# Performance work log

Measured on AMD Instinct MI355X. Metric: run time of the kernel, lower is better.

## Reference

```python
import jax, jax.numpy as jnp
import numpy as np

D_IN = 1024
D_OUT = 1024
N_HEADS = 16

def setup_inputs() -> dict:
    key = jax.random.key(0)
    ks = jax.random.split(key, 6)
    s = 0.02
    return {
        "x": jax.random.normal(ks[0], (4, 2048, D_IN), dtype=jnp.float32),
        "Wq": jax.random.normal(ks[1], (D_IN, D_OUT), dtype=jnp.float32) * s,
        "Wk": jax.random.normal(ks[2], (D_IN, D_OUT), dtype=jnp.float32) * s,
        "Wv": jax.random.normal(ks[3], (D_IN, D_OUT), dtype=jnp.float32) * s,
        "Wo": jax.random.normal(ks[4], (D_OUT, D_OUT), dtype=jnp.float32) * s,
        "bo": jax.random.normal(ks[5], (D_OUT,), dtype=jnp.float32) * s,
    }

def reference(x, Wq, Wk, Wv, Wo, bo):
    b, n, _ = x.shape
    hd = D_OUT // N_HEADS
    # project and split heads -> [b, h, n, hd]
    def split(t):
        return t.reshape(b, n, N_HEADS, hd).transpose(0, 2, 1, 3)
    q = split(x @ Wq)
    k = split(x @ Wk)
    v = split(x @ Wv)
    scores = jnp.einsum('bhqd,bhkd->bhqk', q, k)  # [b,h,n,n]
    causal = jnp.tril(jnp.ones((n, n), dtype=bool))
    scores = jnp.where(causal, scores, -jnp.inf)
    attn = jax.nn.softmax(scores / jnp.sqrt(jnp.float32(hd)), axis=-1)
    ctx = jnp.einsum('bhqk,bhkd->bhqd', attn, v)  # [b,h,n,hd]
    ctx = ctx.transpose(0, 2, 1, 3).reshape(b, n, D_OUT)
    return ctx @ Wo + bo
```

## Files before the change

kernel.cpp:

```cpp
#include <hip/hip_runtime.h>
#include <stdint.h>

typedef unsigned short u16;
typedef __attribute__((ext_vector_type(8))) short frag8;
typedef __attribute__((ext_vector_type(4))) float f32x4;
typedef __attribute__((ext_vector_type(4))) unsigned short u16x4;

#define MFMA_BF16(a,b,c) __builtin_amdgcn_mfma_f32_16x16x32_bf16((a),(b),(c),0,0,0)
#define SMSCALE 0.18033688011112042f

__device__ __forceinline__ u16 f2bf(float f) {
  union { float f; uint32_t u; } c; c.f = f;
  uint32_t u = c.u;
  uint32_t r = (u + 0x7fffu + ((u >> 16) & 1u)) >> 16;
  return (u16)r;
}

__device__ __forceinline__ uint32_t pack_bf16(float a, float b) {
  uint32_t au = __float_as_uint(a) + 0x8000u;
  uint32_t bu = __float_as_uint(b) + 0x8000u;
  return __builtin_amdgcn_perm(bu, au, 0x07060302u);
}

__device__ __forceinline__ void async16(const void* g, void* l) {
  __builtin_amdgcn_global_load_lds((const __attribute__((address_space(1))) void*)g,
                                   (__attribute__((address_space(3))) void*)l,
                                   16, 0, 0);
}

__global__ __launch_bounds__(256) void k_convert_x(const float4* __restrict__ x,
                                                   u16* __restrict__ xb) {
  int i = blockIdx.x * 256 + threadIdx.x;
  float4 v = x[i];
  u16x4 o;
  o.x = f2bf(v.x); o.y = f2bf(v.y); o.z = f2bf(v.z); o.w = f2bf(v.w);
  *(u16x4*)(xb + (size_t)i * 4) = o;
}

__global__ __launch_bounds__(256) void k_transpose_w4(
    const float* __restrict__ W0, const float* __restrict__ W1,
    const float* __restrict__ W2, const float* __restrict__ W3,
    u16* __restrict__ D0, u16* __restrict__ D1,
    u16* __restrict__ D2, u16* __restrict__ D3) {
  __shared__ float tile[64][65];
  const int z = blockIdx.z;
  const float* src = (z == 0) ? W0 : (z == 1) ? W1 : (z == 2) ? W2 : W3;
  u16* dst = (z == 0) ? D0 : (z == 1) ? D1 : (z == 2) ? D2 : D3;
  const int bx = blockIdx.x * 64;
  const int by = blockIdx.y * 64;
  const int t = threadIdx.x;
  const int tc = (t & 15) * 4;
  const int tr = t >> 4;
  #pragma unroll
  for (int p = 0; p < 4; ++p) {
    int r = tr + p * 16;
    float4 v = *(const float4*)(src + (size_t)(bx + r) * 1024 + by + tc);
    tile[r][tc + 0] = v.x; tile[r][tc + 1] = v.y;
    tile[r][tc + 2] = v.z; tile[r][tc + 3] = v.w;
  }
  __syncthreads();
  #pragma unroll
  for (int p = 0; p < 4; ++p) {
    int r = tr + p * 16;
    u16x4 o;
    o.x = f2bf(tile[tc + 0][r]);
    o.y = f2bf(tile[tc + 1][r]);
    o.z = f2bf(tile[tc + 2][r]);
    o.w = f2bf(tile[tc + 3][r]);
    *(u16x4*)(dst + (size_t)(by + r) * 1024 + bx + tc) = o;
  }
}

__global__ __launch_bounds__(256, 2) void k_gemm_qkv(const u16* __restrict__ xb,
    const u16* __restrict__ Wqt, const u16* __restrict__ Wkt, const u16* __restrict__ Wvt,
    u16* __restrict__ Qg, u16* __restrict__ Kg, u16* __restrict__ Vtg) {
  __shared__ __attribute__((aligned(16))) u16 smem[4 * 128 * 64];
  u16* T = smem;
  const int m0 = blockIdx.x * 128, n0 = blockIdx.y * 128;
  const int t = threadIdx.x, lane = t & 63, wv = t >> 6;
  const int lm = lane & 15, quad = lane >> 4;
  const int wr = wv >> 1, wc = wv & 1;
  f32x4 acc[3][4][4] = {};

  for (int k0 = 0; k0 < 1024; k0 += 64) {
    #pragma unroll
    for (int it = 0; it < 4; ++it) {
      int chunk = it * 256 + t;
      int r = chunk >> 3;
      int sc = ((chunk & 7) ^ (r & 7)) * 8;
      async16(xb + (size_t)(m0 + r) * 1024 + k0 + sc,
              smem + (size_t)(it * 256 + wv * 64) * 8);
    }
    #pragma unroll
    for (int z = 0; z < 3; ++z) {
      const u16* Bt = (z == 0) ? Wqt : (z == 1) ? Wkt : Wvt;
      #pragma unroll
      for (int it = 0; it < 4; ++it) {
        int chunk = it * 256 + t;
        int r = chunk >> 3;
        int sc = ((chunk & 7) ^ (r & 7)) * 8;
        async16(Bt + (size_t)(n0 + r) * 1024 + k0 + sc,
                smem + (size_t)((z + 1) * 1024 + it * 256 + wv * 64) * 8);
      }
    }
    __syncthreads();
    #pragma unroll
    for (int kk = 0; kk < 2; ++kk) {
      frag8 a[4];
      #pragma unroll
      for (int i = 0; i < 4; ++i) {
        int row = wr * 64 + i * 16 + lm;
        a[i] = *(const frag8*)(smem + row * 64 + (((kk * 4 + quad) ^ (row & 7)) * 8));
      }
      #pragma unroll
      for (int z = 0; z < 3; ++z) {
        #pragma unroll
        for (int j = 0; j < 4; ++j) {
          int row = wc * 64 + j * 16 + lm;
          frag8 b = *(const frag8*)(smem + (z + 1) * 8192 + row * 64 +
                                    (((kk * 4 + quad) ^ (row & 7)) * 8));
          #pragma unroll
          for (int i = 0; i < 4; ++i)
            acc[z][i][j] = MFMA_BF16(a[i], b, acc[z][i][j]);
        }
      }
    }
    __syncthreads();
  }

  #pragma unroll
  for (int z = 0; z < 2; ++z) {
    u16* tgt = z ? Kg : Qg;
    const float sc = z ? 1.0f : SMSCALE;
    #pragma unroll
    for (int i = 0; i < 4; ++i)
      #pragma unroll
      for (int j = 0; j < 4; ++j) {
        const int col = n0 + wc * 64 + j * 16 + lm;
        const int h = col >> 6, d = col & 63;
        #pragma unroll
        for (int reg = 0; reg < 4; ++reg) {
          const int row = m0 + wr * 64 + i * 16 + quad * 4 + reg;
          const int bb = row >> 11, nn = row & 2047;
          tgt[(((size_t)bb * 16 + h) * 2048 + nn) * 64 + d] = f2bf(acc[z][i][j][reg] * sc);
        }
      }
  }
  {
    const int bb = m0 >> 11, nn0 = m0 & 2047;
    const int h0 = n0 >> 6;
    #pragma unroll
    for (int p = 0; p < 2; ++p) {
      if (wc == p) {
        #pragma unroll
        for (int i = 0; i < 4; ++i)
          #pragma unroll
          for (int j = 0; j < 4; ++j) {
            const int rT = j * 16 + lm;
            #pragma unroll
            for (int reg = 0; reg < 4; ++reg) {
              const int cT = wr * 64 + i * 16 + quad * 4 + reg;
              T[rT * 136 + cT] = f2bf(acc[2][i][j][reg]);
            }
          }
      }
      __syncthreads();
      #pragma unroll
      for (int cc = 0; cc < 4; ++cc) {
        int chunk = cc * 256 + t;
        int r = chunk >> 4, tk = (chunk & 15) * 8;
        frag8 v = *(const frag8*)(T + r * 136 + tk);
        *(frag8*)(Vtg + (((size_t)bb * 16 + h0 + p) * 64 + r) * 2048 + nn0 + tk) = v;
      }
      __syncthreads();
    }
  }
}

__device__ __forceinline__ void attn_tile(const u16* Ks, const u16* Vts, u16* PsW,
                                          const frag8 aq[2], f32x4 o[4], float& l_run,
                                          int lm, int quad, int wv, bool diag) {
  f32x4 s[4];
  #pragma unroll
  for (int kt = 0; kt < 4; ++kt) {
    f32x4 z = {0.f, 0.f, 0.f, 0.f};
    #pragma unroll
    for (int dd = 0; dd < 2; ++dd) {
      frag8 ak = *(const frag8*)(Ks + (kt * 16 + lm) * 64 + (((dd * 4 + quad) ^ (lm & 7)) * 8));
      z = MFMA_BF16(ak, aq[dd], z);
    }
    s[kt] = z;
  }
  if (diag) {
    #pragma unroll
    for (int kt = 0; kt < 4; ++kt)
      #pragma unroll
      for (int rg = 0; rg < 4; ++rg)
        if (kt * 16 + quad * 4 + rg > wv * 16 + lm) s[kt][rg] = -3.0e38f;
  }
  float rs = 0.f;
  #pragma unroll
  for (int kt = 0; kt < 4; ++kt) {
    float p0 = exp2f(s[kt][0]);
    float p1 = exp2f(s[kt][1]);
    float p2 = exp2f(s[kt][2]);
    float p3 = exp2f(s[kt][3]);
    rs += (p0 + p1) + (p2 + p3);
    *(uint32_t*)(PsW + lm * 72 + kt * 16 + quad * 4)     = pack_bf16(p0, p1);
    *(uint32_t*)(PsW + lm * 72 + kt * 16 + quad * 4 + 2) = pack_bf16(p2, p3);
  }
  l_run += rs;
  #pragma unroll
  for (int ks = 0; ks < 2; ++ks) {
    frag8 bp = *(const frag8*)(PsW + lm * 72 + ks * 32 + quad * 8);
    #pragma unroll
    for (int dt = 0; dt < 4; ++dt) {
      frag8 av = *(const frag8*)(Vts + (dt * 16 + lm) * 64 + (((ks * 4 + quad) ^ (lm & 7)) * 8));
      o[dt] = MFMA_BF16(av, bp, o[dt]);
    }
  }
}

__global__ __launch_bounds__(256, 5) void k_attn(const u16* __restrict__ Qg,
                                                 const u16* __restrict__ Kg,
                                                 const u16* __restrict__ Vtg,
                                                 u16* __restrict__ ctx) {
  __shared__ __attribute__((aligned(16))) u16 Ks[64 * 64];
  __shared__ __attribute__((aligned(16))) u16 Vts[64 * 64];
  __shared__ __attribute__((aligned(16))) u16 Ps[4 * 16 * 72];
  const int bid = blockIdx.x;
  const int pair = bid >> 6;
  const int bh = ((bid >> 3) & 7) * 8 + (bid & 7);
  const int t = threadIdx.x, lane = t & 63, wv = t >> 6;
  const int lm = lane & 15, quad = lane >> 4;
  const int b = bh >> 4, h = bh & 15;
  u16* const PsW = Ps + wv * (16 * 72);

  #pragma unroll
  for (int phase = 0; phase < 2; ++phase) {
    const int qt = phase ? (31 - pair) : pair;

    frag8 aq[2];
    {
      const u16* qp = Qg + ((size_t)bh * 2048 + qt * 64 + wv * 16 + lm) * 64 + quad * 8;
      aq[0] = *(const frag8*)(qp);
      aq[1] = *(const frag8*)(qp + 32);
    }
    float l = 0.f;
    f32x4 o[4] = {};

    for (int kt0 = 0; kt0 <= qt; ++kt0) {
      #pragma unroll
      for (int it = 0; it < 2; ++it) {
        int chunk = it * 256 + t;
        int r = chunk >> 3, c = chunk & 7;
        int sc = (c ^ (r & 7)) * 8;
        async16(Kg  + ((size_t)bh * 2048 + kt0 * 64 + r) * 64 + sc, Ks  + (size_t)(it * 256 + wv * 64) * 8);
        async16(Vtg + ((size_t)bh * 64 + r) * 2048 + kt0 * 64 + sc, Vts + (size_t)(it * 256 + wv * 64) * 8);
      }
      __syncthreads();
      attn_tile(Ks, Vts, PsW, aq, o, l, lm, quad, wv, kt0 == qt);
      __syncthreads();
    }

    l += __shfl_xor(l, 16);
    l += __shfl_xor(l, 32);
    const float inv = 1.0f / l;
    #pragma unroll
    for (int dt = 0; dt < 4; ++dt) {
      *(uint32_t*)(PsW + lm * 72 + dt * 16 + quad * 4)     = pack_bf16(o[dt][0] * inv, o[dt][1] * inv);
      *(uint32_t*)(PsW + lm * 72 + dt * 16 + quad * 4 + 2) = pack_bf16(o[dt][2] * inv, o[dt][3] * inv);
    }
    const int rr = lane >> 2, cc = (lane & 3) * 8;
    const size_t row = (size_t)b * 2048 + qt * 64 + wv * 16 + rr;
    #pragma unroll
    for (int half = 0; half < 2; ++half) {
      frag8 vo = *(const frag8*)(PsW + rr * 72 + cc + half * 32);
      *(frag8*)(ctx + row * 1024 + h * 64 + cc + half * 32) = vo;
    }
  }
}

__global__ __launch_bounds__(256) void k_gemm_out(const u16* __restrict__ ctx,
    const u16* __restrict__ Wot, const float* __restrict__ bo, float* __restrict__ out) {
  __shared__ __attribute__((aligned(16))) u16 As[128 * 64];
  __shared__ __attribute__((aligned(16))) u16 Bs[128 * 64];
  const int m0 = blockIdx.x * 128, n0 = blockIdx.y * 128;
  const int t = threadIdx.x, lane = t & 63, wv = t >> 6;
  const int lm = lane & 15, quad = lane >> 4;
  const int wr = wv >> 1, wc = wv & 1;
  f32x4 acc[4][4] = {};
  for (int k0 = 0; k0 < 1024; k0 += 64) {
    #pragma unroll
    for (int it = 0; it < 4; ++it) {
      int chunk = it * 256 + t;
      int r = chunk >> 3;
      int sc = ((chunk & 7) ^ (r & 7)) * 8;
      async16(ctx + (size_t)(m0 + r) * 1024 + k0 + sc, As + (size_t)(it * 256 + wv * 64) * 8);
      async16(Wot + (size_t)(n0 + r) * 1024 + k0 + sc, Bs + (size_t)(it * 256 + wv * 64) * 8);
    }
    __syncthreads();
    #pragma unroll
    for (int kk = 0; kk < 2; ++kk) {
      frag8 a[4];
      #pragma unroll
      for (int i = 0; i < 4; ++i) {
        int row = wr * 64 + i * 16 + lm;
        a[i] = *(const frag8*)(As + row * 64 + (((kk * 4 + quad) ^ (row & 7)) * 8));
      }
      #pragma unroll
      for (int j = 0; j < 4; ++j) {
        int row = wc * 64 + j * 16 + lm;
        frag8 b = *(const frag8*)(Bs + row * 64 + (((kk * 4 + quad) ^ (row & 7)) * 8));
        #pragma unroll
        for (int i = 0; i < 4; ++i)
          acc[i][j] = MFMA_BF16(a[i], b, acc[i][j]);
      }
    }
    __syncthreads();
  }
  #pragma unroll
  for (int i = 0; i < 4; ++i)
    #pragma unroll
    for (int j = 0; j < 4; ++j) {
      const int col = n0 + wc * 64 + j * 16 + lm;
      const float bias = bo[col];
      #pragma unroll
      for (int reg = 0; reg < 4; ++reg) {
        const int row = m0 + wr * 64 + i * 16 + quad * 4 + reg;
        out[(size_t)row * 1024 + col] = acc[i][j][reg] + bias;
      }
    }
}

extern "C" void kernel_launch(void* const* d_in, const int* in_sizes, int n_in,
                              void* d_out, int out_size, void* d_ws, size_t ws_size,
                              hipStream_t stream) {
  const float* x  = (const float*)d_in[0];
  const float* Wq = (const float*)d_in[1];
  const float* Wk = (const float*)d_in[2];
  const float* Wv = (const float*)d_in[3];
  const float* Wo = (const float*)d_in[4];
  const float* bo = (const float*)d_in[5];
  float* out = (float*)d_out;
  char* ws = (char*)d_ws;

  u16* xb   = (u16*)(ws);
  u16* Wqt  = (u16*)(ws + ((size_t)16 << 20));
  u16* Wkt  = (u16*)(ws + ((size_t)18 << 20));
  u16* Wvt  = (u16*)(ws + ((size_t)20 << 20));
  u16* Wot  = (u16*)(ws + ((size_t)22 << 20));
  u16* Qg   = (u16*)(ws + ((size_t)24 << 20));
  u16* Kg   = (u16*)(ws + ((size_t)40 << 20));
  u16* Vtg  = (u16*)(ws + ((size_t)56 << 20));
  u16* ctxb = (u16*)(ws + ((size_t)72 << 20));

  k_convert_x<<<8192, 256, 0, stream>>>((const float4*)x, xb);
  k_transpose_w4<<<dim3(16, 16, 4), 256, 0, stream>>>(Wq, Wk, Wv, Wo, Wqt, Wkt, Wvt, Wot);
  k_gemm_qkv<<<dim3(64, 8), 256, 0, stream>>>(xb, Wqt, Wkt, Wvt, Qg, Kg, Vtg);
  k_attn<<<1024, 256, 0, stream>>>(Qg, Kg, Vtg, ctxb);
  k_gemm_out<<<dim3(64, 8), 256, 0, stream>>>(ctxb, Wot, bo, out);
}
```

Before: 238.1 us.

## Process four query tiles per attention block with double-buffered K/V staging

Each attention block now handles four query tiles (two from the start and two from the end of the causal range) and shares every staged K/V tile among them, so K/V loads and LDS fragment reads are reused across queries. K/V staging is double-buffered so the next tile loads while the current one is computed, leaving one barrier per iteration. The grid is halved to 512 blocks and launch bounds drop to 2 blocks per CU, trading occupancy and more registers (four sets of Q fragments and accumulators) for data reuse and overlap.

Measured after the change: 232.9 us. 2.2% less time.

```diff
diff --git a/kernel.cpp b/kernel.cpp
--- a/kernel.cpp
+++ b/kernel.cpp
@@ -177,102 +177,128 @@
   }
 }
 
-__device__ __forceinline__ void attn_tile(const u16* Ks, const u16* Vts, u16* PsW,
-                                          const frag8 aq[2], f32x4 o[4], float& l_run,
-                                          int lm, int quad, int wv, bool diag) {
-  f32x4 s[4];
-  #pragma unroll
-  for (int kt = 0; kt < 4; ++kt) {
-    f32x4 z = {0.f, 0.f, 0.f, 0.f};
-    #pragma unroll
-    for (int dd = 0; dd < 2; ++dd) {
-      frag8 ak = *(const frag8*)(Ks + (kt * 16 + lm) * 64 + (((dd * 4 + quad) ^ (lm & 7)) * 8));
-      z = MFMA_BF16(ak, aq[dd], z);
-    }
-    s[kt] = z;
-  }
-  if (diag) {
-    #pragma unroll
-    for (int kt = 0; kt < 4; ++kt)
-      #pragma unroll
-      for (int rg = 0; rg < 4; ++rg)
-        if (kt * 16 + quad * 4 + rg > wv * 16 + lm) s[kt][rg] = -3.0e38f;
-  }
-  float rs = 0.f;
-  #pragma unroll
-  for (int kt = 0; kt < 4; ++kt) {
-    float p0 = exp2f(s[kt][0]);
-    float p1 = exp2f(s[kt][1]);
-    float p2 = exp2f(s[kt][2]);
-    float p3 = exp2f(s[kt][3]);
-    rs += (p0 + p1) + (p2 + p3);
-    *(uint32_t*)(PsW + lm * 72 + kt * 16 + quad * 4)     = pack_bf16(p0, p1);
-    *(uint32_t*)(PsW + lm * 72 + kt * 16 + quad * 4 + 2) = pack_bf16(p2, p3);
-  }
-  l_run += rs;
-  #pragma unroll
-  for (int ks = 0; ks < 2; ++ks) {
-    frag8 bp = *(const frag8*)(PsW + lm * 72 + ks * 32 + quad * 8);
-    #pragma unroll
-    for (int dt = 0; dt < 4; ++dt) {
-      frag8 av = *(const frag8*)(Vts + (dt * 16 + lm) * 64 + (((ks * 4 + quad) ^ (lm & 7)) * 8));
-      o[dt] = MFMA_BF16(av, bp, o[dt]);
-    }
-  }
-}
-
-__global__ __launch_bounds__(256, 5) void k_attn(const u16* __restrict__ Qg,
+__global__ __launch_bounds__(256, 2) void k_attn(const u16* __restrict__ Qg,
                                                  const u16* __restrict__ Kg,
                                                  const u16* __restrict__ Vtg,
                                                  u16* __restrict__ ctx) {
-  __shared__ __attribute__((aligned(16))) u16 Ks[64 * 64];
-  __shared__ __attribute__((aligned(16))) u16 Vts[64 * 64];
+  __shared__ __attribute__((aligned(16))) u16 Ks[2][64 * 64];
+  __shared__ __attribute__((aligned(16))) u16 Vts[2][64 * 64];
   __shared__ __attribute__((aligned(16))) u16 Ps[4 * 16 * 72];
   const int bid = blockIdx.x;
-  const int pair = bid >> 6;
+  const int ib = bid >> 6;
   const int bh = ((bid >> 3) & 7) * 8 + (bid & 7);
+  const int qts[4] = {2 * ib, 2 * ib + 1, 30 - 2 * ib, 31 - 2 * ib};
   const int t = threadIdx.x, lane = t & 63, wv = t >> 6;
   const int lm = lane & 15, quad = lane >> 4;
   const int b = bh >> 4, h = bh & 15;
   u16* const PsW = Ps + wv * (16 * 72);
 
-  #pragma unroll
-  for (int phase = 0; phase < 2; ++phase) {
-    const int qt = phase ? (31 - pair) : pair;
-
-    frag8 aq[2];
-    {
-      const u16* qp = Qg + ((size_t)bh * 2048 + qt * 64 + wv * 16 + lm) * 64 + quad * 8;
-      aq[0] = *(const frag8*)(qp);
-      aq[1] = *(const frag8*)(qp + 32);
-    }
-    float l = 0.f;
-    f32x4 o[4] = {};
-
-    for (int kt0 = 0; kt0 <= qt; ++kt0) {
-      #pragma unroll
-      for (int it = 0; it < 2; ++it) {
-        int chunk = it * 256 + t;
-        int r = chunk >> 3, c = chunk & 7;
-        int sc = (c ^ (r & 7)) * 8;
-        async16(Kg  + ((size_t)bh * 2048 + kt0 * 64 + r) * 64 + sc, Ks  + (size_t)(it * 256 + wv * 64) * 8);
-        async16(Vtg + ((size_t)bh * 64 + r) * 2048 + kt0 * 64 + sc, Vts + (size_t)(it * 256 + wv * 64) * 8);
-      }
-      __syncthreads();
-      attn_tile(Ks, Vts, PsW, aq, o, l, lm, quad, wv, kt0 == qt);
-      __syncthreads();
-    }
-
-    l += __shfl_xor(l, 16);
-    l += __shfl_xor(l, 32);
-    const float inv = 1.0f / l;
+  frag8 aq[4][2];
+  #pragma unroll
+  for (int qa = 0; qa < 4; ++qa) {
+    const u16* qp = Qg + ((size_t)bh * 2048 + qts[qa] * 64 + wv * 16 + lm) * 64 + quad * 8;
+    aq[qa][0] = *(const frag8*)(qp);
+    aq[qa][1] = *(const frag8*)(qp + 32);
+  }
+  f32x4 o[4][4] = {};
+  float l[4] = {0.f, 0.f, 0.f, 0.f};
+  const int nst = 32 - 2 * ib;
+
+  auto stage = [&](int kt, int buf) {
+    #pragma unroll
+    for (int it = 0; it < 2; ++it) {
+      int chunk = it * 256 + t;
+      int r = chunk >> 3, c = chunk & 7;
+      int sc = (c ^ (r & 7)) * 8;
+      async16(Kg  + ((size_t)bh * 2048 + kt * 64 + r) * 64 + sc, &Ks[buf][(it * 256 + wv * 64) * 8]);
+      async16(Vtg + ((size_t)bh * 64 + r) * 2048 + kt * 64 + sc,  &Vts[buf][(it * 256 + wv * 64) * 8]);
+    }
+  };
+
+  stage(0, 0);
+  for (int kt0 = 0; kt0 < nst; ++kt0) {
+    const int cur = kt0 & 1;
+    __syncthreads();
+    if (kt0 + 1 < nst) stage(kt0 + 1, cur ^ 1);
+
+    frag8 kf[8];
+    #pragma unroll
+    for (int kt = 0; kt < 4; ++kt)
+      #pragma unroll
+      for (int dd = 0; dd < 2; ++dd)
+        kf[kt * 2 + dd] = *(const frag8*)(&Ks[cur][(kt * 16 + lm) * 64 + (((dd * 4 + quad) ^ (lm & 7)) * 8)]);
+
+    uint32_t pk[4][8];
+    #pragma unroll
+    for (int qa = 0; qa < 4; ++qa) {
+      if (qts[qa] < kt0) continue;
+      f32x4 s[4];
+      #pragma unroll
+      for (int kt = 0; kt < 4; ++kt) {
+        f32x4 z = {0.f, 0.f, 0.f, 0.f};
+        z = MFMA_BF16(kf[kt * 2 + 0], aq[qa][0], z);
+        z = MFMA_BF16(kf[kt * 2 + 1], aq[qa][1], z);
+        s[kt] = z;
+      }
+      if (kt0 == qts[qa]) {
+        #pragma unroll
+        for (int kt = 0; kt < 4; ++kt)
+          #pragma unroll
+          for (int rg = 0; rg < 4; ++rg)
+            if (kt * 16 + quad * 4 + rg > wv * 16 + lm) s[kt][rg] = -3.0e38f;
+      }
+      float rs = 0.f;
+      #pragma unroll
+      for (int kt = 0; kt < 4; ++kt) {
+        float p0 = exp2f(s[kt][0]);
+        float p1 = exp2f(s[kt][1]);
+        float p2 = exp2f(s[kt][2]);
+        float p3 = exp2f(s[kt][3]);
+        rs += (p0 + p1) + (p2 + p3);
+        pk[qa][kt * 2 + 0] = pack_bf16(p0, p1);
+        pk[qa][kt * 2 + 1] = pack_bf16(p2, p3);
+      }
+      l[qa] += rs;
+    }
+
+    frag8 vf[8];
+    #pragma unroll
+    for (int dt = 0; dt < 4; ++dt)
+      #pragma unroll
+      for (int ks = 0; ks < 2; ++ks)
+        vf[dt * 2 + ks] = *(const frag8*)(&Vts[cur][(dt * 16 + lm) * 64 + (((ks * 4 + quad) ^ (lm & 7)) * 8)]);
+
+    #pragma unroll
+    for (int qa = 0; qa < 4; ++qa) {
+      if (qts[qa] < kt0) continue;
+      #pragma unroll
+      for (int kt = 0; kt < 4; ++kt) {
+        *(uint32_t*)(PsW + lm * 72 + kt * 16 + quad * 4)     = pk[qa][kt * 2 + 0];
+        *(uint32_t*)(PsW + lm * 72 + kt * 16 + quad * 4 + 2) = pk[qa][kt * 2 + 1];
+      }
+      #pragma unroll
+      for (int ks = 0; ks < 2; ++ks) {
+        frag8 bp = *(const frag8*)(PsW + lm * 72 + ks * 32 + quad * 8);
+        #pragma unroll
+        for (int dt = 0; dt < 4; ++dt)
+          o[qa][dt] = MFMA_BF16(vf[dt * 2 + ks], bp, o[qa][dt]);
+      }
+    }
+  }
+
+  #pragma unroll
+  for (int qa = 0; qa < 4; ++qa) {
+    float lv = l[qa];
+    lv += __shfl_xor(lv, 16);
+    lv += __shfl_xor(lv, 32);
+    const float inv = 1.0f / lv;
     #pragma unroll
     for (int dt = 0; dt < 4; ++dt) {
-      *(uint32_t*)(PsW + lm * 72 + dt * 16 + quad * 4)     = pack_bf16(o[dt][0] * inv, o[dt][1] * inv);
-      *(uint32_t*)(PsW + lm * 72 + dt * 16 + quad * 4 + 2) = pack_bf16(o[dt][2] * inv, o[dt][3] * inv);
+      *(uint32_t*)(PsW + lm * 72 + dt * 16 + quad * 4)     = pack_bf16(o[qa][dt][0] * inv, o[qa][dt][1] * inv);
+      *(uint32_t*)(PsW + lm * 72 + dt * 16 + quad * 4 + 2) = pack_bf16(o[qa][dt][2] * inv, o[qa][dt][3] * inv);
     }
     const int rr = lane >> 2, cc = (lane & 3) * 8;
-    const size_t row = (size_t)b * 2048 + qt * 64 + wv * 16 + rr;
+    const size_t row = (size_t)b * 2048 + qts[qa] * 64 + wv * 16 + rr;
     #pragma unroll
     for (int half = 0; half < 2; ++half) {
       frag8 vo = *(const frag8*)(PsW + rr * 72 + cc + half * 32);
@@ -358,6 +384,6 @@
   k_convert_x<<<8192, 256, 0, stream>>>((const float4*)x, xb);
   k_transpose_w4<<<dim3(16, 16, 4), 256, 0, stream>>>(Wq, Wk, Wv, Wo, Wqt, Wkt, Wvt, Wot);
   k_gemm_qkv<<<dim3(64, 8), 256, 0, stream>>>(xb, Wqt, Wkt, Wvt, Qg, Kg, Vtg);
-  k_attn<<<1024, 256, 0, stream>>>(Qg, Kg, Vtg, ctxb);
+  k_attn<<<512, 256, 0, stream>>>(Qg, Kg, Vtg, ctxb);
   k_gemm_out<<<dim3(64, 8), 256, 0, stream>>>(ctxb, Wot, bo, out);
 }
```
